# Kernel optimization log

Hardware: AMD Instinct MI355X
Metric: run time of the kernel (lower is better)

The kernel has to match this reference:

```python
import jax, jax.numpy as jnp
import numpy as np

NORMALIZED_LENGTH = 512  # init kwarg
T_FRAMES = 32768
N_LM = 543  # mediapipe holistic landmark count


def setup_inputs() -> dict:
    key = jax.random.key(0)
    kf, kn, kd, ki = jax.random.split(key, 4)
    frames = jax.random.uniform(kf, (T_FRAMES, N_LM, 3), dtype=jnp.float32)
    nan_mask = jax.random.uniform(kn, (T_FRAMES, N_LM, 3)) < 0.10
    frames = jnp.where(nan_mask, jnp.float32(jnp.nan), frames)
    drop = jax.random.uniform(kd, (T_FRAMES,)) < 0.05
    hand_zone = jnp.arange(N_LM) >= 468
    frames = jnp.where(drop[:, None, None] & hand_zone[None, :, None], jnp.float32(jnp.nan), frames)
    lips_idx = jax.random.randint(ki, (40,), 0, 468, dtype=jnp.int32)
    return {"frames": frames, "lips_idx": lips_idx}


def _nan_mean0(x):
    # tf_nan_mean over axis 0 (keepdims); 0/0 -> NaN in TF is immediately zeroed
    # afterwards, so we emit 0 directly (identical forward values, safe grads).
    finite = ~jnp.isnan(x)
    s = jnp.where(finite, x, jnp.zeros((), x.dtype)).sum(axis=0, keepdims=True)
    c = finite.sum(axis=0, keepdims=True)
    return jnp.where(c == 0, jnp.zeros((), x.dtype), s / jnp.maximum(c, 1).astype(x.dtype))


def reference(frames, lips_idx):
    fr = frames[:, :, :2]                       # drop z coord
    lh = fr[:, 468:489]                         # [T, 21, 2]
    rh = fr[:, 522:543]                         # [T, 21, 2]
    lh = jnp.stack([lh[..., 0], 1.0 - lh[..., 1]], axis=-1)
    rh = jnp.stack([1.0 - rh[..., 0], 1.0 - rh[..., 1]], axis=-1)
    # stack hands, NaN->0, sum over the 2-hand axis
    hand = jnp.nan_to_num(lh) + jnp.nan_to_num(rh)   # [T, 21, 2]
    keep = hand.sum(axis=(1, 2)) != 0.0              # frames with >=1 visible hand
    hand = hand[keep]                                # [S, 21, 2]
    lips = fr[:, lips_idx][keep]                     # [S, 40, 2]
    lips = jnp.where(jnp.isnan(lips), _nan_mean0(lips), lips)
    raw = jnp.concatenate([hand, lips], axis=1)      # [S, 61, 2]
    S = int(raw.shape[0])
    # tf.linspace(0, S-1, L+1) cast to int32 -> segment boundaries (truncation)
    b = np.linspace(0.0, S - 1.0, NORMALIZED_LENGTH + 1).astype(np.int32)
    # frame t belongs to bin i with b[i] <= t < b[i+1]; t >= b[L] maps to L (dropped)
    seg = jnp.asarray(np.searchsorted(b, np.arange(S), side="right") - 1)
    sums = jax.ops.segment_sum(raw, seg, num_segments=NORMALIZED_LENGTH)
    cnt = jax.ops.segment_sum(jnp.ones((S,), raw.dtype), seg, num_segments=NORMALIZED_LENGTH)
    # raw is NaN-free at this point, so nan-mean == plain mean; empty bin -> NaN -> 0
    mean = jnp.where(cnt[:, None, None] == 0, jnp.zeros((), raw.dtype),
                     sums / jnp.maximum(cnt, 1.0)[:, None, None])
    sampled = mean.reshape(NORMALIZED_LENGTH, -1)    # Flatten -> [L, 122]
    rows = sampled.sum(axis=1) != 0.0                # drop all-zero (empty) bins
    return sampled[rows]
```

## Files before the change

### kernel.cpp

```cpp
#include <hip/hip_runtime.h>

#define T_FRAMES 32768
#define ROWF 1629
#define NSEG 512
#define NVAL 122
#define STRIDE 128
#define PADI 16

__global__ __launch_bounds__(1024) void k1_keep_stats(
    const float* __restrict__ frames, const int* __restrict__ lips_idx,
    int* __restrict__ keep, float* __restrict__ lip_sum,
    int* __restrict__ lip_cnt, float* __restrict__ stage) {
  __shared__ float ls[80];
  __shared__ int lc[80];
  int tid = threadIdx.x;
  if (tid < 80) { ls[tid] = 0.0f; lc[tid] = 0; }
  __syncthreads();

  int lane = tid & 63;
  int wid = tid >> 6;
  int t = blockIdx.x * 16 + wid;
  const float* f = frames + (size_t)t * ROWF;
  float* srow = stage + (size_t)t * STRIDE;

  float hv = 0.0f;
  if (lane < 42) {
    int j = lane >> 1, c = lane & 1;
    float lh = f[(468 + j) * 3 + c];
    float rh = f[(522 + j) * 3 + c];
    float a = (c == 0) ? lh : (1.0f - lh);
    float b = 1.0f - rh;
    a = (a == a) ? a : 0.0f;
    b = (b == b) ? b : 0.0f;
    hv = a + b;
    srow[lane] = hv;
  }
  float s = hv;
  #pragma unroll
  for (int off = 32; off > 0; off >>= 1) s += __shfl_down(s, off);
  s = __shfl(s, 0);
  int kp = (s != 0.0f) ? 1 : 0;
  if (lane == 0) keep[t] = kp;

  #pragma unroll
  for (int p = 0; p < 2; ++p) {
    int v = lane + p * 64;
    if (v < 80) {
      int j = v >> 1, c = v & 1;
      float x = f[lips_idx[j] * 3 + c];
      srow[42 + v] = x;
      if (kp && (x == x)) {
        atomicAdd(&ls[v], x);
        atomicAdd(&lc[v], 1);
      }
    }
  }
  __syncthreads();
  if (tid < 80) {
    atomicAdd(&lip_sum[tid * PADI], ls[tid]);
    atomicAdd(&lip_cnt[tid * PADI], lc[tid]);
  }
}

__global__ __launch_bounds__(1024) void k2_scan(const int* __restrict__ keep,
                                                int* __restrict__ kept_t,
                                                int* __restrict__ Sp) {
  __shared__ int wsum[16];
  int tid = threadIdx.x;
  const int PER = T_FRAMES / 1024;
  int base = tid * PER;
  int fl[PER];
  int local = 0;
  #pragma unroll
  for (int k = 0; k < PER; ++k) { fl[k] = keep[base + k]; local += fl[k]; }

  int lane = tid & 63, wid = tid >> 6;
  int scan = local;
  #pragma unroll
  for (int off = 1; off < 64; off <<= 1) {
    int n = __shfl_up(scan, off);
    if (lane >= off) scan += n;
  }
  if (lane == 63) wsum[wid] = scan;
  __syncthreads();
  if (tid < 16) {
    int v = wsum[tid];
    #pragma unroll
    for (int off = 1; off < 16; off <<= 1) {
      int n = __shfl_up(v, off);
      if (tid >= off) v += n;
    }
    wsum[tid] = v;
  }
  __syncthreads();
  int excl = ((wid == 0) ? 0 : wsum[wid - 1]) + (scan - local);
  #pragma unroll
  for (int k = 0; k < PER; ++k) {
    if (fl[k]) kept_t[excl++] = base + k;
  }
  if (tid == 1023) Sp[0] = wsum[15];
}

__global__ __launch_bounds__(512) void k3_segments(
    const float* __restrict__ stage, const int* __restrict__ kept_t,
    const int* __restrict__ Sp, const float* __restrict__ lip_sum,
    const int* __restrict__ lip_cnt, float* __restrict__ out, int out_size) {
  __shared__ int seglist[128];
  __shared__ float part[4][128];
  int tid = threadIdx.x;
  int v = tid & 127;
  int r = tid >> 7;
  int seg = blockIdx.x;
  long long Sm1 = (long long)Sp[0] - 1;
  if (Sm1 < 0) Sm1 = 0;
  int lo = (int)(((long long)seg * Sm1) >> 9);
  int hi = (int)(((long long)(seg + 1) * Sm1) >> 9);
  int cnt = hi - lo;

  for (int k = tid; k < cnt; k += 512) seglist[k] = kept_t[lo + k];
  __syncthreads();

  float cm = 0.0f;
  if (v >= 42 && v < NVAL) {
    int w = v - 42;
    int c = lip_cnt[w * PADI];
    cm = (c == 0) ? 0.0f : lip_sum[w * PADI] / (float)c;
  }

  float acc = 0.0f;
  if (v < NVAL) {
    for (int k = r; k < cnt; k += 4) {
      float x = stage[(size_t)seglist[k] * STRIDE + v];
      acc += (x == x) ? x : cm;
    }
  }
  part[r][v] = acc;
  __syncthreads();
  if (r == 0 && v < NVAL) {
    float tot = part[0][v] + part[1][v] + part[2][v] + part[3][v];
    float mean = (cnt == 0) ? 0.0f : tot / (float)cnt;
    int o = seg * NVAL + v;
    if (o < out_size) out[o] = mean;
  }
}

extern "C" void kernel_launch(void* const* d_in, const int* in_sizes, int n_in,
                              void* d_out, int out_size, void* d_ws, size_t ws_size,
                              hipStream_t stream) {
  const float* frames = (const float*)d_in[0];
  const int* lips_idx = (const int*)d_in[1];
  float* out = (float*)d_out;

  char* ws = (char*)d_ws;
  int* keep      = (int*)(ws);
  int* kept_t    = (int*)(ws + 131072);
  int* Sp        = (int*)(ws + 262144);
  float* lip_sum = (float*)(ws + 262208);
  int* lip_cnt   = (int*)(ws + 267328);
  float* stage   = (float*)(ws + 274432);

  hipMemsetAsync((void*)lip_sum, 0, 10240, stream);

  k1_keep_stats<<<2048, 1024, 0, stream>>>(frames, lips_idx, keep, lip_sum,
                                           lip_cnt, stage);
  k2_scan<<<1, 1024, 0, stream>>>(keep, kept_t, Sp);
  k3_segments<<<NSEG, 512, 0, stream>>>(stage, kept_t, Sp, lip_sum, lip_cnt,
                                        out, out_size);
}
```

Before: 317.6 us.

## Drop staging buffer; read frames directly per segment with algebraic lip-mean fill

The first kernel now only computes the per-frame keep flag, using smaller blocks, and no longer writes a staged copy of hand and lip values or accumulates lip statistics. The segment kernel reads kept frames straight from the input and accumulates hand sums plus per-segment lip sums and finite counts. A new final kernel fills NaN lips algebraically as (sum + (n - count) * global_mean) / n. This removes the staging write and re-read pass, but adds a kernel launch, uses more scattered gathers from the frame rows, and needs special handling for the dropped trailing frame.

```diff
diff --git a/kernel.cpp b/kernel.cpp
--- a/kernel.cpp
+++ b/kernel.cpp
@@ -4,62 +4,29 @@
 #define ROWF 1629
 #define NSEG 512
 #define NVAL 122
-#define STRIDE 128
 #define PADI 16
 
-__global__ __launch_bounds__(1024) void k1_keep_stats(
-    const float* __restrict__ frames, const int* __restrict__ lips_idx,
-    int* __restrict__ keep, float* __restrict__ lip_sum,
-    int* __restrict__ lip_cnt, float* __restrict__ stage) {
-  __shared__ float ls[80];
-  __shared__ int lc[80];
-  int tid = threadIdx.x;
-  if (tid < 80) { ls[tid] = 0.0f; lc[tid] = 0; }
-  __syncthreads();
-
-  int lane = tid & 63;
-  int wid = tid >> 6;
-  int t = blockIdx.x * 16 + wid;
+__global__ __launch_bounds__(256) void k1_keep(const float* __restrict__ frames,
+                                               int* __restrict__ keep) {
+  int lane = threadIdx.x & 63;
+  int wid = threadIdx.x >> 6;
+  int t = blockIdx.x * 4 + wid;
   const float* f = frames + (size_t)t * ROWF;
-  float* srow = stage + (size_t)t * STRIDE;
-
-  float hv = 0.0f;
+  float s = 0.0f;
   if (lane < 42) {
-    int j = lane >> 1, c = lane & 1;
-    float lh = f[(468 + j) * 3 + c];
-    float rh = f[(522 + j) * 3 + c];
-    float a = (c == 0) ? lh : (1.0f - lh);
-    float b = 1.0f - rh;
-    a = (a == a) ? a : 0.0f;
-    b = (b == b) ? b : 0.0f;
-    hv = a + b;
-    srow[lane] = hv;
-  }
-  float s = hv;
+    int j = (lane < 21) ? lane : lane - 21;
+    int base = ((lane < 21) ? 468 : 522) + j;
+    float x = f[base * 3];
+    float y = f[base * 3 + 1];
+    float ax = (lane < 21) ? x : 1.0f - x;
+    float ay = 1.0f - y;
+    ax = (ax == ax) ? ax : 0.0f;
+    ay = (ay == ay) ? ay : 0.0f;
+    s = ax + ay;
+  }
   #pragma unroll
   for (int off = 32; off > 0; off >>= 1) s += __shfl_down(s, off);
-  s = __shfl(s, 0);
-  int kp = (s != 0.0f) ? 1 : 0;
-  if (lane == 0) keep[t] = kp;
-
-  #pragma unroll
-  for (int p = 0; p < 2; ++p) {
-    int v = lane + p * 64;
-    if (v < 80) {
-      int j = v >> 1, c = v & 1;
-      float x = f[lips_idx[j] * 3 + c];
-      srow[42 + v] = x;
-      if (kp && (x == x)) {
-        atomicAdd(&ls[v], x);
-        atomicAdd(&lc[v], 1);
-      }
-    }
-  }
-  __syncthreads();
-  if (tid < 80) {
-    atomicAdd(&lip_sum[tid * PADI], ls[tid]);
-    atomicAdd(&lip_cnt[tid * PADI], lc[tid]);
-  }
+  if (lane == 0) keep[t] = (s != 0.0f) ? 1 : 0;
 }
 
 __global__ __launch_bounds__(1024) void k2_scan(const int* __restrict__ keep,
@@ -101,47 +68,120 @@
   if (tid == 1023) Sp[0] = wsum[15];
 }
 
-__global__ __launch_bounds__(512) void k3_segments(
-    const float* __restrict__ stage, const int* __restrict__ kept_t,
-    const int* __restrict__ Sp, const float* __restrict__ lip_sum,
-    const int* __restrict__ lip_cnt, float* __restrict__ out, int out_size) {
-  __shared__ int seglist[128];
-  __shared__ float part[4][128];
-  int tid = threadIdx.x;
-  int v = tid & 127;
-  int r = tid >> 7;
+__global__ __launch_bounds__(1024) void k3_seg(
+    const float* __restrict__ frames, const int* __restrict__ lips_idx,
+    const int* __restrict__ kept_t, const int* __restrict__ Sp,
+    float* __restrict__ out, int out_size,
+    float* __restrict__ seg_ls, int* __restrict__ seg_lc,
+    int* __restrict__ seg_n, float* __restrict__ tot_s,
+    int* __restrict__ tot_c) {
+  __shared__ int seglist[72];
+  __shared__ float h_s[42];
+  __shared__ float l_s[80];
+  __shared__ int   l_c[80];
+  int tid = threadIdx.x, lane = tid & 63, wid = tid >> 6;
   int seg = blockIdx.x;
-  long long Sm1 = (long long)Sp[0] - 1;
-  if (Sm1 < 0) Sm1 = 0;
-  int lo = (int)(((long long)seg * Sm1) >> 9);
-  int hi = (int)(((long long)(seg + 1) * Sm1) >> 9);
+  int S = Sp[0];
+  long long M = (long long)S - 1; if (M < 0) M = 0;
+  int lo = (int)(((long long)seg * M) >> 9);
+  int hi = (int)(((long long)(seg + 1) * M) >> 9);
   int cnt = hi - lo;
-
-  for (int k = tid; k < cnt; k += 512) seglist[k] = kept_t[lo + k];
-  __syncthreads();
-
-  float cm = 0.0f;
-  if (v >= 42 && v < NVAL) {
-    int w = v - 42;
-    int c = lip_cnt[w * PADI];
-    cm = (c == 0) ? 0.0f : lip_sum[w * PADI] / (float)c;
-  }
-
-  float acc = 0.0f;
-  if (v < NVAL) {
-    for (int k = r; k < cnt; k += 4) {
-      float x = stage[(size_t)seglist[k] * STRIDE + v];
-      acc += (x == x) ? x : cm;
+  int loadN = cnt + ((seg == NSEG - 1 && S >= 2) ? 1 : 0);
+
+  if (tid < 42) h_s[tid] = 0.0f;
+  if (tid < 80) { l_s[tid] = 0.0f; l_c[tid] = 0; }
+  if (tid < loadN) seglist[tid] = kept_t[lo + tid];
+  __syncthreads();
+
+  int idx1 = 0, idx2 = 0;
+  if (lane >= 42) idx1 = lips_idx[lane - 42];
+  if (lane < 18)  idx2 = lips_idx[22 + lane];
+
+  float ahx = 0.0f, ahy = 0.0f;
+  float a1x = 0.0f, a1y = 0.0f; int c1x = 0, c1y = 0;
+  float a2x = 0.0f, a2y = 0.0f; int c2x = 0, c2y = 0;
+
+  for (int k = wid; k < cnt; k += 16) {
+    const float* f = frames + (size_t)seglist[k] * ROWF;
+    int o1;
+    if (lane < 21)      o1 = (468 + lane) * 3;
+    else if (lane < 42) o1 = (522 + (lane - 21)) * 3;
+    else                o1 = idx1 * 3;
+    float x1 = f[o1], y1 = f[o1 + 1];
+    float x2 = 0.0f, y2 = 0.0f;
+    if (lane < 18) { int o2 = idx2 * 3; x2 = f[o2]; y2 = f[o2 + 1]; }
+
+    float ax = (lane < 21) ? x1 : 1.0f - x1;
+    float ay = 1.0f - y1;
+    ax = (ax == ax) ? ax : 0.0f;
+    ay = (ay == ay) ? ay : 0.0f;
+    float bx = __shfl(ax, lane + 21);
+    float by = __shfl(ay, lane + 21);
+    if (lane < 21) { ahx += ax + bx; ahy += ay + by; }
+    if (lane >= 42) {
+      if (x1 == x1) { a1x += x1; c1x++; }
+      if (y1 == y1) { a1y += y1; c1y++; }
     }
-  }
-  part[r][v] = acc;
-  __syncthreads();
-  if (r == 0 && v < NVAL) {
-    float tot = part[0][v] + part[1][v] + part[2][v] + part[3][v];
-    float mean = (cnt == 0) ? 0.0f : tot / (float)cnt;
-    int o = seg * NVAL + v;
-    if (o < out_size) out[o] = mean;
-  }
+    if (lane < 18) {
+      if (x2 == x2) { a2x += x2; c2x++; }
+      if (y2 == y2) { a2y += y2; c2y++; }
+    }
+  }
+
+  if (lane < 21) { atomicAdd(&h_s[2 * lane], ahx); atomicAdd(&h_s[2 * lane + 1], ahy); }
+  if (lane >= 42) {
+    int j = lane - 42;
+    atomicAdd(&l_s[2 * j], a1x); atomicAdd(&l_s[2 * j + 1], a1y);
+    atomicAdd(&l_c[2 * j], c1x); atomicAdd(&l_c[2 * j + 1], c1y);
+  }
+  if (lane < 18) {
+    int j = 22 + lane;
+    atomicAdd(&l_s[2 * j], a2x); atomicAdd(&l_s[2 * j + 1], a2y);
+    atomicAdd(&l_c[2 * j], c2x); atomicAdd(&l_c[2 * j + 1], c2y);
+  }
+  __syncthreads();
+
+  if (tid < 42) {
+    float v = cnt ? h_s[tid] / (float)cnt : 0.0f;
+    int o = seg * NVAL + tid;
+    if (o < out_size) out[o] = v;
+  }
+  if (tid < 80) {
+    seg_ls[seg * 80 + tid] = l_s[tid];
+    seg_lc[seg * 80 + tid] = l_c[tid];
+    atomicAdd(&tot_s[tid * PADI], l_s[tid]);
+    atomicAdd(&tot_c[tid * PADI], l_c[tid]);
+  }
+  if (tid == 0) seg_n[seg] = cnt;
+
+  if (seg == NSEG - 1 && S >= 2 && wid == 0 && lane < 40) {
+    const float* f = frames + (size_t)seglist[cnt] * ROWF;
+    int idx = lips_idx[lane];
+    float x = f[idx * 3], y = f[idx * 3 + 1];
+    if (x == x) { atomicAdd(&tot_s[(2 * lane) * PADI], x);
+                  atomicAdd(&tot_c[(2 * lane) * PADI], 1); }
+    if (y == y) { atomicAdd(&tot_s[(2 * lane + 1) * PADI], y);
+                  atomicAdd(&tot_c[(2 * lane + 1) * PADI], 1); }
+  }
+}
+
+__global__ __launch_bounds__(128) void k4_final(
+    const float* __restrict__ seg_ls, const int* __restrict__ seg_lc,
+    const int* __restrict__ seg_n, const float* __restrict__ tot_s,
+    const int* __restrict__ tot_c, float* __restrict__ out, int out_size) {
+  int w = threadIdx.x;
+  int seg = blockIdx.x;
+  if (w >= 80) return;
+  int tc = tot_c[w * PADI];
+  float cm = tc ? tot_s[w * PADI] / (float)tc : 0.0f;
+  int n = seg_n[seg];
+  float v = 0.0f;
+  if (n) {
+    int c = seg_lc[seg * 80 + w];
+    v = (seg_ls[seg * 80 + w] + (float)(n - c) * cm) / (float)n;
+  }
+  int o = seg * NVAL + 42 + w;
+  if (o < out_size) out[o] = v;
 }
 
 extern "C" void kernel_launch(void* const* d_in, const int* in_sizes, int n_in,
@@ -155,15 +195,18 @@
   int* keep      = (int*)(ws);
   int* kept_t    = (int*)(ws + 131072);
   int* Sp        = (int*)(ws + 262144);
-  float* lip_sum = (float*)(ws + 262208);
-  int* lip_cnt   = (int*)(ws + 267328);
-  float* stage   = (float*)(ws + 274432);
-
-  hipMemsetAsync((void*)lip_sum, 0, 10240, stream);
-
-  k1_keep_stats<<<2048, 1024, 0, stream>>>(frames, lips_idx, keep, lip_sum,
-                                           lip_cnt, stage);
+  float* tot_s   = (float*)(ws + 262208);
+  int* tot_c     = (int*)(ws + 267328);
+  float* seg_ls  = (float*)(ws + 272448);
+  int* seg_lc    = (int*)(ws + 436288);
+  int* seg_n     = (int*)(ws + 600128);
+
+  hipMemsetAsync((void*)tot_s, 0, 10240, stream);
+
+  k1_keep<<<8192, 256, 0, stream>>>(frames, keep);
   k2_scan<<<1, 1024, 0, stream>>>(keep, kept_t, Sp);
-  k3_segments<<<NSEG, 512, 0, stream>>>(stage, kept_t, Sp, lip_sum, lip_cnt,
-                                        out, out_size);
-}
+  k3_seg<<<NSEG, 1024, 0, stream>>>(frames, lips_idx, kept_t, Sp, out, out_size,
+                                    seg_ls, seg_lc, seg_n, tot_s, tot_c);
+  k4_final<<<NSEG, 128, 0, stream>>>(seg_ls, seg_lc, seg_n, tot_s, tot_c,
+                                     out, out_size);
+}
```

Measured after the change: 300.7 us. 1.06x faster.
